# Kernel tuning notes

Hardware: AMD Instinct MI355X
Metric: run time of the kernel (lower is better)

Reference implementation:

```python
import jax, jax.numpy as jnp
import numpy as np

D = 1024
H = 16
N = 4096
D_K = D // H
SCALE = D_K ** 0.5


def setup_inputs() -> dict:
    key = jax.random.key(0)
    k_x, k_w = jax.random.split(key)
    X = jax.random.normal(k_x, (N, D), dtype=jnp.float32)
    # nn.Linear(D, 2*D, bias=False): weight [2D, D], y = X @ W.T
    Wqkv = jax.random.normal(k_w, (2 * D, D), dtype=jnp.float32) * (1.0 / np.sqrt(D))
    return {"X": X, "Wqkv": Wqkv}


def reference(X, Wqkv):
    n = X.shape[0]
    proj = X @ Wqkv.T                      # [N, 2D]
    qk, v = jnp.split(proj, 2, axis=-1)    # each [N, D]
    qk = qk.reshape(n, H, D_K)             # [N, H, d_k]
    v = v.reshape(n, H, D_K)
    s = jnp.einsum('nhd,mhd->hnm', qk, qk) / SCALE  # [H, N, N]
    a = jax.nn.softmax(s, axis=-1)
    ctx = jnp.einsum('hnm,mhd->nhd', a, v).reshape(n, H * D_K)
    return ctx
```

## Files before the change

### kernel.cpp

```cpp
#include <hip/hip_runtime.h>
#include <hip/hip_bf16.h>

#define N_TOK   4096
#define D_MODEL 1024
#define H_HEADS 16
#define DK      64
#define KVB     64
#define QK_PRESCALE 0.42466092f

#define PC_HALF_STRIDE  (4096u * 1024u)
#define PL_HALF_STRIDE  (4096u * 16u)
#define WS_NEED (16u*1024u*1024u + 33u*1024u*1024u)

typedef float  f32x4   __attribute__((ext_vector_type(4)));
typedef float  f32x16  __attribute__((ext_vector_type(16)));
typedef short  bf16x8  __attribute__((ext_vector_type(8)));

__device__ __forceinline__ ushort f2bf(float f) {
  union { float f; unsigned u; } v; v.f = f;
  unsigned u = v.u;
  u += 0x7fffu + ((u >> 16) & 1u);
  return (ushort)(u >> 16);
}

__device__ __forceinline__ unsigned cvt_pk_bf16(float lo, float hi) {
  unsigned r;
  asm("v_cvt_pk_bf16_f32 %0, %1, %2" : "=v"(r) : "v"(lo), "v"(hi));
  return r;
}

__device__ __forceinline__ float exp2_raw(float x) {
  float r;
  asm("v_exp_f32 %0, %1" : "=v"(r) : "v"(x));
  return r;
}

__device__ __forceinline__ void gload_lds16(const void* gsrc, void* ldst) {
  __builtin_amdgcn_global_load_lds(
      (const __attribute__((address_space(1))) unsigned int*)gsrc,
      (__attribute__((address_space(3))) unsigned int*)ldst, 16, 0, 0);
}

__device__ __forceinline__ f32x16 mfma32(bf16x8 a, bf16x8 b, f32x16 c) {
  return __builtin_amdgcn_mfma_f32_32x32x16_bf16(a, b, c, 0, 0, 0);
}

__device__ __forceinline__ void swap32(unsigned &a, unsigned &b) {
  asm("v_permlane32_swap_b32 %0, %1" : "+v"(a), "+v"(b));
}

__global__ __launch_bounds__(256) void cvt_bf16_kernel(
    const float* __restrict__ X, const float* __restrict__ W,
    ushort* __restrict__ Xb, ushort* __restrict__ Wb) {
  const size_t i = (size_t)blockIdx.x * 256 + threadIdx.x;
  const float* s;
  ushort* d;
  size_t off;
  if (i < 524288) { s = X; d = Xb; off = i * 8; }
  else            { s = W; d = Wb; off = (i - 524288) * 8; }
  float4 a = *(const float4*)(s + off);
  float4 b = *(const float4*)(s + off + 4);
  ushort4 lo, hi;
  lo.x = f2bf(a.x); lo.y = f2bf(a.y); lo.z = f2bf(a.z); lo.w = f2bf(a.w);
  hi.x = f2bf(b.x); hi.y = f2bf(b.y); hi.z = f2bf(b.z); hi.w = f2bf(b.w);
  *(ushort4*)(d + off)     = lo;
  *(ushort4*)(d + off + 4) = hi;
}

__global__ __launch_bounds__(256) void qkv_gemm_kernel(
    const ushort* __restrict__ Xb, const ushort* __restrict__ Wb,
    ushort* __restrict__ Qb, ushort* __restrict__ Vt) {
  __shared__ ushort As[2][128][32];
  __shared__ ushort Bs[2][128][32];

  const int tid  = threadIdx.x;
  const int lane = tid & 63;
  const int g    = lane >> 4;
  const int lr   = lane & 15;
  const int wave = tid >> 6;
  const int wr   = (wave >> 1) * 64;
  const int wc   = (wave & 1) * 64;

  const int bid = blockIdx.x;
  const int x   = bid & 7;
  const int i   = bid >> 3;
  const int rb  = (x >> 1) * 8 + (i >> 3);
  const int cb  = (x & 1) * 8 + (i & 7);

  f32x4 acc[4][4] = {};

  const int r0 = tid >> 2;
  const int c0 = (tid & 3) * 8;
  const ushort* xsrc = Xb + (size_t)(rb * 128 + r0) * D_MODEL + c0;
  const ushort* wsrc = Wb + (size_t)(cb * 128 + r0) * D_MODEL + c0;

#define GST(BUF, K0)                                                         \
  {                                                                          \
    gload_lds16(xsrc + (K0), (ushort*)As[BUF] + tid * 8);                    \
    gload_lds16(xsrc + 64 * D_MODEL + (K0), (ushort*)As[BUF] + (tid + 256) * 8); \
    gload_lds16(wsrc + (K0), (ushort*)Bs[BUF] + tid * 8);                    \
    gload_lds16(wsrc + 64 * D_MODEL + (K0), (ushort*)Bs[BUF] + (tid + 256) * 8); \
  }

  GST(0, 0);
  __syncthreads();

  for (int k0 = 0; k0 < D_MODEL; k0 += 32) {
    const int buf = (k0 >> 5) & 1;
    if (k0 + 32 < D_MODEL) GST(buf ^ 1, k0 + 32);

    bf16x8 a[4], b[4];
#pragma unroll
    for (int m = 0; m < 4; ++m) a[m] = *(const bf16x8*)&As[buf][wr + m * 16 + lr][g * 8];
#pragma unroll
    for (int n = 0; n < 4; ++n) b[n] = *(const bf16x8*)&Bs[buf][wc + n * 16 + lr][g * 8];

#pragma unroll
    for (int m = 0; m < 4; ++m)
#pragma unroll
      for (int n = 0; n < 4; ++n)
        acc[m][n] = __builtin_amdgcn_mfma_f32_16x16x32_bf16(a[m], b[n], acc[m][n], 0, 0, 0);
    __syncthreads();
  }

  const int nrow0 = rb * 128 + wr;
  const int jcol0 = cb * 128 + wc;
  if (cb < 8) {
#pragma unroll
    for (int m = 0; m < 4; ++m) {
      const int nn = nrow0 + m * 16 + 4 * g;
#pragma unroll
      for (int n = 0; n < 4; ++n) {
        const int j = jcol0 + n * 16 + lr;
#pragma unroll
        for (int r = 0; r < 4; ++r)
          Qb[(size_t)(nn + r) * D_MODEL + j] = f2bf(acc[m][n][r] * QK_PRESCALE);
      }
    }
  } else {
#pragma unroll
    for (int m = 0; m < 4; ++m) {
      const int nn = nrow0 + m * 16 + 4 * g;
#pragma unroll
      for (int n = 0; n < 4; ++n) {
        const int c = jcol0 - D_MODEL + n * 16 + lr;
        uint2 pv = { cvt_pk_bf16(acc[m][n][0], acc[m][n][1]),
                     cvt_pk_bf16(acc[m][n][2], acc[m][n][3]) };
        *(uint2*)(Vt + (size_t)c * N_TOK + nn) = pv;
      }
    }
  }
}

template <int SPLIT>
__global__ __launch_bounds__(512, 4) void attn_kernel(
    const ushort* __restrict__ Qb, const ushort* __restrict__ Vg,
    float* __restrict__ OutOrPc, float* __restrict__ Pl) {
  __shared__ ushort Kt[2][64][64];
  __shared__ ushort Vt[2][64][64];

  const int tid  = threadIdx.x;
  const int lane = tid & 63;
  const int l31  = lane & 31;
  const int hi   = lane >> 5;
  const int wave = tid >> 6;

  const int bid = blockIdx.x;
  int h, qbase, half, kvlo, nit;
  if constexpr (SPLIT) {
    const int i = bid >> 3;
    h     = (bid & 7) * 2 + (i >> 5);
    half  = (i >> 4) & 1;
    qbase = (i & 15) * 256 + wave * 32;
    kvlo  = half * (N_TOK / 2);
    nit   = (N_TOK / 2) / KVB;
  } else {
    const int i = bid >> 3;
    h     = (bid & 7) * 2 + (i >> 4);
    half  = 0;
    qbase = (i & 15) * 256 + wave * 32;
    kvlo  = 0;
    nit   = N_TOK / KVB;
  }

  bf16x8 qf[4];
  const ushort* qrow = Qb + (size_t)(qbase + l31) * D_MODEL + h * DK;
#pragma unroll
  for (int ks = 0; ks < 4; ++ks)
    qf[ks] = *(const bf16x8*)(qrow + ks * 16 + hi * 8);

  float l_run = 0.f;
  const f32x16 zz = {};
  f32x16 ctx0 = {}, ctx1 = {};

  const int srow = tid >> 3;
  const int scg  = (tid & 7) ^ (srow & 7);
  const ushort* kst = Qb + (size_t)(kvlo + srow) * D_MODEL + h * DK + scg * 8;
  const ushort* vst = Vg + (size_t)(h * DK + srow) * N_TOK + kvlo + scg * 8;

#define STAGE_ADV(BUF)                                                        \
  {                                                                           \
    gload_lds16(kst, (ushort*)Kt[BUF] + (size_t)tid * 8);                     \
    gload_lds16(vst, (ushort*)Vt[BUF] + (size_t)tid * 8);                     \
    kst += (size_t)KVB * D_MODEL;                                             \
    vst += KVB;                                                               \
  }

#define ATTN_BODY(BUF)                                                        \
  {                                                                           \
    if (stages_left > 0) { STAGE_ADV(BUF ^ 1); --stages_left; }               \
    f32x16 st0 = zz, st1 = zz;                                                \
    __builtin_amdgcn_s_setprio(1);                                            \
    _Pragma("unroll")                                                         \
    for (int ks = 0; ks < 4; ++ks) {                                          \
      bf16x8 kf0 = *(const bf16x8*)&Kt[BUF][l31][((((ks << 1) | hi)) ^ (l31 & 7)) << 3]; \
      bf16x8 kf1 = *(const bf16x8*)&Kt[BUF][32 + l31][((((ks << 1) | hi)) ^ (l31 & 7)) << 3]; \
      st0 = mfma32(kf0, qf[ks], st0);                                         \
      st1 = mfma32(kf1, qf[ks], st1);                                         \
    }                                                                         \
    __builtin_amdgcn_s_setprio(0);                                            \
    float rsb[4];                                                             \
    unsigned pk0[8], pk1[8];                                                  \
    _Pragma("unroll")                                                         \
    for (int b = 0; b < 4; ++b) {                                             \
      float a0 = exp2_raw(st0[4 * b + 0]);                                    \
      float a1 = exp2_raw(st0[4 * b + 1]);                                    \
      float a2 = exp2_raw(st0[4 * b + 2]);                                    \
      float a3 = exp2_raw(st0[4 * b + 3]);                                    \
      float c0 = exp2_raw(st1[4 * b + 0]);                                    \
      float c1 = exp2_raw(st1[4 * b + 1]);                                    \
      float c2 = exp2_raw(st1[4 * b + 2]);                                    \
      float c3 = exp2_raw(st1[4 * b + 3]);                                    \
      rsb[b] = ((a0 + a1) + (a2 + a3)) + ((c0 + c1) + (c2 + c3));             \
      pk0[2 * b]     = cvt_pk_bf16(a0, a1);                                   \
      pk0[2 * b + 1] = cvt_pk_bf16(a2, a3);                                   \
      pk1[2 * b]     = cvt_pk_bf16(c0, c1);                                   \
      pk1[2 * b + 1] = cvt_pk_bf16(c2, c3);                                   \
    }                                                                         \
    l_run += (rsb[0] + rsb[1]) + (rsb[2] + rsb[3]);                           \
    _Pragma("unroll")                                                         \
    for (int kt = 0; kt < 2; ++kt) {                                          \
      _Pragma("unroll")                                                       \
      for (int km = 0; km < 2; ++km) {                                        \
        unsigned u0 = kt ? pk1[4 * km + 0] : pk0[4 * km + 0];                 \
        unsigned u1 = kt ? pk1[4 * km + 1] : pk0[4 * km + 1];                 \
        unsigned u2 = kt ? pk1[4 * km + 2] : pk0[4 * km + 2];                 \
        unsigned u3 = kt ? pk1[4 * km + 3] : pk0[4 * km + 3];                 \
        swap32(u0, u2);                                                       \
        swap32(u1, u3);                                                       \
        union { unsigned u[4]; bf16x8 v; } pf;                                \
        pf.u[0] = u0; pf.u[1] = u1; pf.u[2] = u2; pf.u[3] = u3;               \
        const int ck = (kt << 2) | (km << 1) | hi;                            \
        bf16x8 vf0 = *(const bf16x8*)&Vt[BUF][l31][(ck ^ (l31 & 7)) << 3];    \
        bf16x8 vf1 = *(const bf16x8*)&Vt[BUF][32 + l31][(ck ^ (l31 & 7)) << 3]; \
        __builtin_amdgcn_s_setprio(1);                                        \
        ctx0 = mfma32(vf0, pf.v, ctx0);                                       \
        ctx1 = mfma32(vf1, pf.v, ctx1);                                       \
        __builtin_amdgcn_s_setprio(0);                                        \
      }                                                                       \
    }                                                                         \
    __syncthreads();                                                          \
  }

  int stages_left = nit - 1;
  STAGE_ADV(0);
  __syncthreads();

  for (int it = 0; it < nit; it += 2) {
    ATTN_BODY(0);
    ATTN_BODY(1);
  }

  l_run += __shfl_xor(l_run, 32);

  if constexpr (SPLIT) {
    float* pc = OutOrPc + (size_t)half * PC_HALF_STRIDE
              + (size_t)(qbase + l31) * D_MODEL + h * DK;
#pragma unroll
    for (int r = 0; r < 16; ++r) {
      const int d = (r & 3) + 8 * (r >> 2) + 4 * hi;
      pc[d]      = ctx0[r];
      pc[32 + d] = ctx1[r];
    }
    if (hi == 0)
      Pl[(size_t)half * PL_HALF_STRIDE + (size_t)(qbase + l31) * H_HEADS + h] = l_run;
  } else {
    const float inv = 1.f / l_run;
    float* orow = OutOrPc + (size_t)(qbase + l31) * D_MODEL + h * DK;
#pragma unroll
    for (int r = 0; r < 16; ++r) {
      const int d = (r & 3) + 8 * (r >> 2) + 4 * hi;
      orow[d]      = ctx0[r] * inv;
      orow[32 + d] = ctx1[r] * inv;
    }
  }
}

__global__ __launch_bounds__(256) void combine_kernel(
    const float* __restrict__ Pc, const float* __restrict__ Pl,
    float* __restrict__ Out) {
  const unsigned quad = blockIdx.x * 256 + threadIdx.x;
  const unsigned q = quad >> 8;
  const unsigned h = (quad >> 4) & 15;

  const float l0 = Pl[(size_t)q * H_HEADS + h];
  const float l1 = Pl[PL_HALF_STRIDE + (size_t)q * H_HEADS + h];
  const float w  = 1.f / (l0 + l1);

  const float4 c0 = *(const float4*)(Pc + (size_t)quad * 4);
  const float4 c1 = *(const float4*)(Pc + PC_HALF_STRIDE + (size_t)quad * 4);
  float4 o;
  o.x = (c0.x + c1.x) * w;
  o.y = (c0.y + c1.y) * w;
  o.z = (c0.z + c1.z) * w;
  o.w = (c0.w + c1.w) * w;
  *(float4*)(Out + (size_t)quad * 4) = o;
}

extern "C" void kernel_launch(void* const* d_in, const int* in_sizes, int n_in,
                              void* d_out, int out_size, void* d_ws, size_t ws_size,
                              hipStream_t stream) {
  const float* X = (const float*)d_in[0];
  const float* W = (const float*)d_in[1];
  float* Out = (float*)d_out;

  ushort* Qb = (ushort*)d_ws;
  ushort* Vt = Qb + (size_t)N_TOK * D_MODEL;
  float*  Pc = (float*)((char*)d_ws + 16u * 1024u * 1024u);
  float*  Pl = (float*)((char*)d_ws + 48u * 1024u * 1024u);
  ushort* Xb = (ushort*)Pc;
  ushort* Wb = Xb + (size_t)N_TOK * D_MODEL;

  cvt_bf16_kernel<<<dim3(3072), dim3(256), 0, stream>>>(X, W, Xb, Wb);

  qkv_gemm_kernel<<<dim3(512), dim3(256), 0, stream>>>(Xb, Wb, Qb, Vt);

  if (ws_size >= WS_NEED) {
    attn_kernel<1><<<dim3(512), dim3(512), 0, stream>>>(Qb, Vt, Pc, Pl);
    combine_kernel<<<dim3(4096), dim3(256), 0, stream>>>(Pc, Pl, Out);
  } else {
    attn_kernel<0><<<dim3(256), dim3(512), 0, stream>>>(Qb, Vt, Out, nullptr);
  }
}
```

Measured before the change: 128.3 us.

## Replace split-KV attention plus combine with 256-thread full-KV blocks

```diff
diff --git a/kernel.cpp b/kernel.cpp
--- a/kernel.cpp
+++ b/kernel.cpp
@@ -8,9 +8,6 @@
 #define KVB     64
 #define QK_PRESCALE 0.42466092f
 
-#define PC_HALF_STRIDE  (4096u * 1024u)
-#define PL_HALF_STRIDE  (4096u * 16u)
-#define WS_NEED (16u*1024u*1024u + 33u*1024u*1024u)
 
 typedef float  f32x4   __attribute__((ext_vector_type(4)));
 typedef float  f32x16  __attribute__((ext_vector_type(16)));
@@ -152,10 +149,9 @@
   }
 }
 
-template <int SPLIT>
-__global__ __launch_bounds__(512, 4) void attn_kernel(
+__global__ __launch_bounds__(256, 4) void attn_kernel(
     const ushort* __restrict__ Qb, const ushort* __restrict__ Vg,
-    float* __restrict__ OutOrPc, float* __restrict__ Pl) {
+    float* __restrict__ Out) {
   __shared__ ushort Kt[2][64][64];
   __shared__ ushort Vt[2][64][64];
 
@@ -166,22 +162,10 @@
   const int wave = tid >> 6;
 
   const int bid = blockIdx.x;
-  int h, qbase, half, kvlo, nit;
-  if constexpr (SPLIT) {
-    const int i = bid >> 3;
-    h     = (bid & 7) * 2 + (i >> 5);
-    half  = (i >> 4) & 1;
-    qbase = (i & 15) * 256 + wave * 32;
-    kvlo  = half * (N_TOK / 2);
-    nit   = (N_TOK / 2) / KVB;
-  } else {
-    const int i = bid >> 3;
-    h     = (bid & 7) * 2 + (i >> 4);
-    half  = 0;
-    qbase = (i & 15) * 256 + wave * 32;
-    kvlo  = 0;
-    nit   = N_TOK / KVB;
-  }
+  const int i   = bid >> 3;
+  const int h   = (bid & 7) * 2 + (i >> 5);
+  const int qbase = (i & 31) * 128 + wave * 32;
+  const int nit = N_TOK / KVB;
 
   bf16x8 qf[4];
   const ushort* qrow = Qb + (size_t)(qbase + l31) * D_MODEL + h * DK;
@@ -195,13 +179,17 @@
 
   const int srow = tid >> 3;
   const int scg  = (tid & 7) ^ (srow & 7);
-  const ushort* kst = Qb + (size_t)(kvlo + srow) * D_MODEL + h * DK + scg * 8;
-  const ushort* vst = Vg + (size_t)(h * DK + srow) * N_TOK + kvlo + scg * 8;
+  const ushort* kst = Qb + (size_t)srow * D_MODEL + h * DK + scg * 8;
+  const ushort* vst = Vg + (size_t)(h * DK + srow) * N_TOK + scg * 8;
 
 #define STAGE_ADV(BUF)                                                        \
   {                                                                           \
-    gload_lds16(kst, (ushort*)Kt[BUF] + (size_t)tid * 8);                     \
-    gload_lds16(vst, (ushort*)Vt[BUF] + (size_t)tid * 8);                     \
+    ushort* kd = (ushort*)Kt[BUF] + (size_t)tid * 8;                          \
+    ushort* vd = (ushort*)Vt[BUF] + (size_t)tid * 8;                          \
+    gload_lds16(kst, kd);                                                     \
+    gload_lds16(kst + 32 * D_MODEL, kd + 2048);                               \
+    gload_lds16(vst, vd);                                                     \
+    gload_lds16(vst + 32 * N_TOK, vd + 2048);                                 \
     kst += (size_t)KVB * D_MODEL;                                             \
     vst += KVB;                                                               \
   }
@@ -273,48 +261,14 @@
 
   l_run += __shfl_xor(l_run, 32);
 
-  if constexpr (SPLIT) {
-    float* pc = OutOrPc + (size_t)half * PC_HALF_STRIDE
-              + (size_t)(qbase + l31) * D_MODEL + h * DK;
-#pragma unroll
-    for (int r = 0; r < 16; ++r) {
-      const int d = (r & 3) + 8 * (r >> 2) + 4 * hi;
-      pc[d]      = ctx0[r];
-      pc[32 + d] = ctx1[r];
-    }
-    if (hi == 0)
-      Pl[(size_t)half * PL_HALF_STRIDE + (size_t)(qbase + l31) * H_HEADS + h] = l_run;
-  } else {
-    const float inv = 1.f / l_run;
-    float* orow = OutOrPc + (size_t)(qbase + l31) * D_MODEL + h * DK;
-#pragma unroll
-    for (int r = 0; r < 16; ++r) {
-      const int d = (r & 3) + 8 * (r >> 2) + 4 * hi;
-      orow[d]      = ctx0[r] * inv;
-      orow[32 + d] = ctx1[r] * inv;
-    }
-  }
-}
-
-__global__ __launch_bounds__(256) void combine_kernel(
-    const float* __restrict__ Pc, const float* __restrict__ Pl,
-    float* __restrict__ Out) {
-  const unsigned quad = blockIdx.x * 256 + threadIdx.x;
-  const unsigned q = quad >> 8;
-  const unsigned h = (quad >> 4) & 15;
-
-  const float l0 = Pl[(size_t)q * H_HEADS + h];
-  const float l1 = Pl[PL_HALF_STRIDE + (size_t)q * H_HEADS + h];
-  const float w  = 1.f / (l0 + l1);
-
-  const float4 c0 = *(const float4*)(Pc + (size_t)quad * 4);
-  const float4 c1 = *(const float4*)(Pc + PC_HALF_STRIDE + (size_t)quad * 4);
-  float4 o;
-  o.x = (c0.x + c1.x) * w;
-  o.y = (c0.y + c1.y) * w;
-  o.z = (c0.z + c1.z) * w;
-  o.w = (c0.w + c1.w) * w;
-  *(float4*)(Out + (size_t)quad * 4) = o;
+  const float inv = 1.f / l_run;
+  float* orow = Out + (size_t)(qbase + l31) * D_MODEL + h * DK;
+#pragma unroll
+  for (int r = 0; r < 16; ++r) {
+    const int d = (r & 3) + 8 * (r >> 2) + 4 * hi;
+    orow[d]      = ctx0[r] * inv;
+    orow[32 + d] = ctx1[r] * inv;
+  }
 }
 
 extern "C" void kernel_launch(void* const* d_in, const int* in_sizes, int n_in,
@@ -326,19 +280,12 @@
 
   ushort* Qb = (ushort*)d_ws;
   ushort* Vt = Qb + (size_t)N_TOK * D_MODEL;
-  float*  Pc = (float*)((char*)d_ws + 16u * 1024u * 1024u);
-  float*  Pl = (float*)((char*)d_ws + 48u * 1024u * 1024u);
-  ushort* Xb = (ushort*)Pc;
+  ushort* Xb = Vt + (size_t)N_TOK * D_MODEL;
   ushort* Wb = Xb + (size_t)N_TOK * D_MODEL;
 
   cvt_bf16_kernel<<<dim3(3072), dim3(256), 0, stream>>>(X, W, Xb, Wb);
 
   qkv_gemm_kernel<<<dim3(512), dim3(256), 0, stream>>>(Xb, Wb, Qb, Vt);
 
-  if (ws_size >= WS_NEED) {
-    attn_kernel<1><<<dim3(512), dim3(512), 0, stream>>>(Qb, Vt, Pc, Pl);
-    combine_kernel<<<dim3(4096), dim3(256), 0, stream>>>(Pc, Pl, Out);
-  } else {
-    attn_kernel<0><<<dim3(256), dim3(512), 0, stream>>>(Qb, Vt, Out, nullptr);
-  }
-}
+  attn_kernel<<<dim3(512), dim3(256), 0, stream>>>(Qb, Vt, Out);
+}
```

New measurement: 122.1 us. 1.05x faster.
